# Optimization experiments

Hardware: AMD Instinct MI355X
Metric: run time of the kernel (lower is better)

## Reference

```python
import jax, jax.numpy as jnp
from jax import lax
import numpy as np

DIM = 800
FEAT = 192
LAYERS = 5
BLOCK_SZ = [32, 192, 192, 192, 192]
BLOCK_RNG = [0, 32, 224, 416, 608, 800]
HALF = 27  # image_size//4//2 - 1 with image_size=224
EPS = 1e-5


def conv2d(x, w, stride=1, pad=0, groups=1):
    return lax.conv_general_dilated(
        x, w, (stride, stride), [(pad, pad), (pad, pad)],
        dimension_numbers=("NCHW", "OIHW", "NCHW"),
        feature_group_count=groups)


def _bcast(v):
    return v[None, :, None, None]


def setup_inputs() -> dict:
    key = jax.random.key(0)
    ks = jax.random.split(key, 22)
    B = 32
    s = 0.05
    return {
        "x": jax.random.normal(ks[0], (B, 3, 224, 224), jnp.float32),
        "ds_w1": jax.random.normal(ks[1], (16, 3, 3, 3), jnp.float32) * s,
        "ds_b1": jax.random.normal(ks[2], (16,), jnp.float32) * s,
        "bn1_g": jax.random.uniform(ks[3], (16,), jnp.float32) + 0.5,
        "bn1_b": jax.random.normal(ks[4], (16,), jnp.float32) * s,
        "bn1_m": jax.random.normal(ks[5], (16,), jnp.float32) * s,
        "bn1_v": jax.random.uniform(ks[6], (16,), jnp.float32) + 0.5,
        "ds_dw": jax.random.normal(ks[7], (16, 1, 3, 3), jnp.float32) * s,
        "ds_dwb": jax.random.normal(ks[8], (16,), jnp.float32) * s,
        "ds_w2": jax.random.normal(ks[9], (32, 16, 1, 1), jnp.float32) * s,
        "ds_b2": jax.random.normal(ks[10], (32,), jnp.float32) * s,
        "bn2_g": jax.random.uniform(ks[11], (32,), jnp.float32) + 0.5,
        "bn2_b": jax.random.normal(ks[12], (32,), jnp.float32) * s,
        "bn2_m": jax.random.normal(ks[13], (32,), jnp.float32) * s,
        "bn2_v": jax.random.uniform(ks[14], (32,), jnp.float32) + 0.5,
        "conv_dw": jax.random.normal(ks[15], (DIM, 1, 3, 3), jnp.float32) * s,
        "gw": jax.random.normal(ks[16], (DIM, DIM), jnp.float32) * s,
        "in_gamma": jax.random.uniform(ks[17], (DIM,), jnp.float32) + 0.5,
        "in_beta": jax.random.normal(ks[18], (DIM,), jnp.float32) * s,
        "fc_w": jax.random.normal(ks[19], (1000, FEAT), jnp.float32) * s,
        "fc_b": jax.random.normal(ks[20], (1000,), jnp.float32) * s,
    }


def _forward(x, ds_w1, ds_b1, bn1_g, bn1_b, bn1_m, bn1_v, ds_dw, ds_dwb,
             ds_w2, ds_b2, bn2_g, bn2_b, bn2_m, bn2_v, conv_dw, gw,
             in_gamma, in_beta, fc_w, fc_b):
    # ---- downsample stem: conv3x3 s2 -> BN -> ReLU -> dwconv3x3 s2 -> conv1x1 -> BN
    h = conv2d(x, ds_w1, 2, 1) + _bcast(ds_b1)
    h = (h - _bcast(bn1_m)) * _bcast(bn1_g * lax.rsqrt(bn1_v + EPS)) + _bcast(bn1_b)
    h = jax.nn.relu(h)
    h = conv2d(h, ds_dw, 2, 1, groups=16) + _bcast(ds_dwb)
    h = conv2d(h, ds_w2, 1, 0) + _bcast(ds_b2)
    h = (h - _bcast(bn2_m)) * _bcast(bn2_g * lax.rsqrt(bn2_v + EPS)) + _bcast(bn2_b)
    B, _, H, W = h.shape  # (B, 32, 56, 56)
    h = jnp.concatenate([h, jnp.zeros((B, DIM - 32, H, W), h.dtype)], axis=1)

    # ---- per-block InstanceNorm -> ReLU -> depthwise conv -> sliced 1x1 graph conv -> residual
    for i in range(LAYERS):
        s, r0, r1 = BLOCK_SZ[i], BLOCK_RNG[i], BLOCK_RNG[i + 1]
        xa = h[:, :s]
        mu = xa.mean((2, 3), keepdims=True)
        var = ((xa - mu) ** 2).mean((2, 3), keepdims=True)
        xa = (xa - mu) * lax.rsqrt(var + EPS)
        xa = xa * _bcast(in_gamma[r0:r1]) + _bcast(in_beta[r0:r1])
        xa = jax.nn.relu(xa)
        xa = conv2d(xa, conv_dw[r0:r1], 1, 1, groups=s)
        row0 = min(r1, DIM - FEAT)
        xa = jnp.einsum("oc,bchw->bohw", gw[row0:, r0:r1], xa)
        h = (h[:, s:] if i < LAYERS - 1 else h[:, -FEAT:]) + xa

    # ---- AvgPool2d(2) over the 3x3 crop keeps only the top-left 2x2 mean
    out = h[:, :, HALF - 1:HALF + 1, HALF - 1:HALF + 1].mean((2, 3))
    return out @ fc_w.T + fc_b


def reference(x, ds_w1, ds_b1, bn1_g, bn1_b, bn1_m, bn1_v, ds_dw, ds_dwb,
              ds_w2, ds_b2, bn2_g, bn2_b, bn2_m, bn2_v, conv_dw, gw,
              in_gamma, in_beta, fc_w, fc_b):
    return _forward(x, ds_w1, ds_b1, bn1_g, bn1_b, bn1_m, bn1_v, ds_dw, ds_dwb,
                    ds_w2, ds_b2, bn2_g, bn2_b, bn2_m, bn2_v, conv_dw, gw,
                    in_gamma, in_beta, fc_w, fc_b)
```

## Files before the change

kernel.cpp:

```cpp
#include <hip/hip_runtime.h>
#include <stddef.h>

#define EPS 1e-5f
#define N_HW 3136
#define G 16
#define NG (G * N_HW)
#define DIMC 800

typedef unsigned short u16;
typedef __attribute__((ext_vector_type(8))) short short8;
typedef __attribute__((ext_vector_type(4))) float floatx4;

__device__ __forceinline__ u16 f2b(float f) {
  unsigned u = __float_as_uint(f);
  u += 0x7FFFu + ((u >> 16) & 1u);
  return (u16)(u >> 16);
}
__device__ __forceinline__ float blo(unsigned u) { return __uint_as_float(u << 16); }
__device__ __forceinline__ float bhi(unsigned u) { return __uint_as_float(u & 0xFFFF0000u); }

static const size_t XA_OFF  = 0;
static const size_t H0_OFF  = 61014016ull;
static const size_t BLK_OFF = 67436544ull;
static const size_t GWB_OFF = 105971712ull;
static const size_t M4_OFF  = 107251712ull;
static const size_t MH_OFF  = M4_OFF + 192 * G * 4;
static const size_t OP_OFF  = MH_OFF + 192 * G * 4;
static const size_t NEED    = OP_OFF + (size_t)G * 192 * 4;

__global__ __launch_bounds__(256) void gw2bf(const float* __restrict__ gw, u16* __restrict__ gwb) {
  int i = (blockIdx.x * 256 + threadIdx.x) * 4;
  float4 v = *(const float4*)(gw + i);
  gwb[i + 0] = f2b(v.x); gwb[i + 1] = f2b(v.y);
  gwb[i + 2] = f2b(v.z); gwb[i + 3] = f2b(v.w);
}

#define XT_PITCH 226
#define XT_CH (17 * XT_PITCH)
__global__ __launch_bounds__(256) void stem_conv1(
    const float* __restrict__ xg, const float* __restrict__ w, const float* __restrict__ b1,
    const float* __restrict__ g, const float* __restrict__ bb,
    const float* __restrict__ m, const float* __restrict__ v,
    float* __restrict__ h1) {
  __shared__ float xt[3 * XT_CH];
  __shared__ float wt[16 * 27];
  __shared__ float mulc[16], addc[16];
  int blk = blockIdx.x;
  int s = blk % 14;
  int bg = blk / 14;
  int tid = threadIdx.x;

  for (int e = tid; e < 432; e += 256) wt[e] = w[e];
  if (tid < 16) {
    float A = g[tid] * rsqrtf(v[tid] + EPS);
    mulc[tid] = A;
    addc[tid] = (b1[tid] - m[tid]) * A + bb[tid];
  }
  int iy0 = 16 * s - 1;
  for (int e = tid; e < 3 * XT_CH; e += 256) {
    int ci = e / XT_CH;
    int rem = e - ci * XT_CH;
    int r = rem / XT_PITCH;
    int cc = rem - r * XT_PITCH;
    int iy = iy0 + r, ix = cc - 1;
    float val = 0.f;
    if (iy >= 0 && iy < 224 && ix >= 0 && ix < 224)
      val = xg[((size_t)(bg * 3 + ci)) * 224 * 224 + iy * 224 + ix];
    xt[e] = val;
  }
  __syncthreads();

  for (int p = tid; p < 8 * 112; p += 256) {
    int oyl = p / 112, ox = p - oyl * 112;
    float xv[27];
#pragma unroll
    for (int ci = 0; ci < 3; ci++)
#pragma unroll
      for (int ky = 0; ky < 3; ky++)
#pragma unroll
        for (int kx = 0; kx < 3; kx++)
          xv[ci * 9 + ky * 3 + kx] = xt[ci * XT_CH + (2 * oyl + ky) * XT_PITCH + 2 * ox + kx];
    int oy = 8 * s + oyl;
#pragma unroll
    for (int c = 0; c < 16; c++) {
      float acc = 0.f;
#pragma unroll
      for (int t = 0; t < 27; t++) acc += xv[t] * wt[c * 27 + t];
      float y = acc * mulc[c] + addc[c];
      h1[(size_t)(c * G + bg) * 12544 + oy * 112 + ox] = fmaxf(y, 0.f);
    }
  }
}

__global__ __launch_bounds__(256) void stem_dw(
    const float* __restrict__ h1, const float* __restrict__ dw, const float* __restrict__ dwb,
    float* __restrict__ h2) {
  int idx = blockIdx.x * 256 + threadIdx.x;
  int q = idx % N_HW;
  int t = idx / N_HW;
  int bg = t & (G - 1);
  int c = t >> 4;
  int qy = q / 56, qx = q % 56;
  const float* plane = h1 + (size_t)(c * G + bg) * 12544;
  float acc = dwb[c];
#pragma unroll
  for (int ky = 0; ky < 3; ky++) {
    int iy = qy * 2 - 1 + ky;
    if (iy < 0 || iy >= 112) continue;
#pragma unroll
    for (int kx = 0; kx < 3; kx++) {
      int ix = qx * 2 - 1 + kx;
      if (ix < 0 || ix >= 112) continue;
      acc += plane[iy * 112 + ix] * dw[c * 9 + ky * 3 + kx];
    }
  }
  h2[idx] = acc;
}

__global__ __launch_bounds__(256) void stem_pw(
    const float* __restrict__ h2, const float* __restrict__ w2, const float* __restrict__ b2,
    const float* __restrict__ g, const float* __restrict__ bb,
    const float* __restrict__ m, const float* __restrict__ v,
    float* __restrict__ H0) {
  int idx = blockIdx.x * 256 + threadIdx.x;
  int q = idx % N_HW;
  int t = idx / N_HW;
  int bg = t & (G - 1);
  int o = t >> 4;
  float acc = b2[o];
#pragma unroll
  for (int c = 0; c < 16; c++) acc += w2[o * 16 + c] * h2[(size_t)(c * G + bg) * N_HW + q];
  float y = (acc - m[o]) * (g[o] * rsqrtf(v[o] + EPS)) + bb[o];
  H0[idx] = y;
}

template <typename T>
__global__ __launch_bounds__(256) void dw_fused(
    const T* __restrict__ base, const float* __restrict__ cdw,
    const float* __restrict__ in_g, const float* __restrict__ in_b,
    u16* __restrict__ XA, int cdwoff) {
  __shared__ float sm[58 * 58];
  __shared__ float wred[8];
  int blk = blockIdx.x;
  int cl = blk >> 4;
  int c = cdwoff + cl;
  int tid = threadIdx.x;

  if (tid < 58) { sm[tid] = 0.f; sm[57 * 58 + tid] = 0.f; }
  if (tid >= 64 && tid < 120) { int r = tid - 63; sm[r * 58] = 0.f; sm[r * 58 + 57] = 0.f; }

  const T* row = base + (size_t)blk * N_HW;
  float s = 0.f, s2 = 0.f;
  for (int i = tid; i < 392; i += 256) {
    float vals[8];
    if constexpr (sizeof(T) == 2) {
      uint4 u = *(const uint4*)((const u16*)row + i * 8);
      vals[0] = blo(u.x); vals[1] = bhi(u.x);
      vals[2] = blo(u.y); vals[3] = bhi(u.y);
      vals[4] = blo(u.z); vals[5] = bhi(u.z);
      vals[6] = blo(u.w); vals[7] = bhi(u.w);
    } else {
      float4 v0 = *(const float4*)((const float*)row + i * 8);
      float4 v1 = *(const float4*)((const float*)row + i * 8 + 4);
      vals[0] = v0.x; vals[1] = v0.y; vals[2] = v0.z; vals[3] = v0.w;
      vals[4] = v1.x; vals[5] = v1.y; vals[6] = v1.z; vals[7] = v1.w;
    }
    int p = i * 8;
    int y = p / 56, x = p - y * 56;
    float* d = &sm[(y + 1) * 58 + x + 1];
#pragma unroll
    for (int e = 0; e < 8; e++) {
      d[e] = vals[e];
      s += vals[e];
      s2 += vals[e] * vals[e];
    }
  }
#pragma unroll
  for (int o = 32; o > 0; o >>= 1) {
    s += __shfl_down(s, o);
    s2 += __shfl_down(s2, o);
  }
  if ((tid & 63) == 0) { wred[(tid >> 6) * 2] = s; wred[(tid >> 6) * 2 + 1] = s2; }
  __syncthreads();
  float ts = (wred[0] + wred[2]) + (wred[4] + wred[6]);
  float tq = (wred[1] + wred[3]) + (wred[5] + wred[7]);
  float mean = ts * (1.f / N_HW);
  float var = fmaxf(tq * (1.f / N_HW) - mean * mean, 0.f);
  float sc = in_g[c] * rsqrtf(var + EPS);
  float sh = in_b[c] - mean * sc;

  for (int i = tid; i < N_HW; i += 256) {
    int y = i / 56, x = i - y * 56;
    int pos = (y + 1) * 58 + x + 1;
    sm[pos] = fmaxf(sm[pos] * sc + sh, 0.f);
  }
  __syncthreads();

  float w0 = cdw[c * 9 + 0], w1 = cdw[c * 9 + 1], w2 = cdw[c * 9 + 2];
  float w3 = cdw[c * 9 + 3], w4 = cdw[c * 9 + 4], w5 = cdw[c * 9 + 5];
  float w6 = cdw[c * 9 + 6], w7 = cdw[c * 9 + 7], w8 = cdw[c * 9 + 8];
  u16* outp = XA + (size_t)blk * N_HW;
  for (int pp = tid; pp < N_HW / 2; pp += 256) {
    int p = pp * 2;
    int y = p / 56, x = p - y * 56;
    const float* p0 = &sm[y * 58 + x];
    float a0 = p0[0] * w0 + p0[1] * w1 + p0[2] * w2
             + p0[58] * w3 + p0[59] * w4 + p0[60] * w5
             + p0[116] * w6 + p0[117] * w7 + p0[118] * w8;
    float a1 = p0[1] * w0 + p0[2] * w1 + p0[3] * w2
             + p0[59] * w3 + p0[60] * w4 + p0[61] * w5
             + p0[117] * w6 + p0[118] * w7 + p0[119] * w8;
    unsigned pk = (unsigned)f2b(a0) | ((unsigned)f2b(a1) << 16);
    *(unsigned*)&outp[p] = pk;
  }
}

template <typename TC>
__global__ __launch_bounds__(256) void gemm_mfma(
    const u16* __restrict__ A, const u16* __restrict__ B, TC* __restrict__ C, int K) {
  __shared__ u16 As[2][192][40];
  __shared__ u16 Bs[2][32][64];
  int n0 = blockIdx.x * 64;
  int tid = threadIdx.x;
  int wave = tid >> 6, lane = tid & 63;
  int wm = wave >> 1, wn = wave & 1;
  int lg = lane >> 4, li = lane & 15;
  floatx4 acc[6][2] = {};

  int ar = tid >> 2, ak = (tid & 3) * 8;
  int bk = tid >> 3, bn = (tid & 7) * 8;
  int bnx = bn ^ ((bk >> 3) << 4);
  const u16* Ag = A + (size_t)ar * DIMC + ak;
  const u16* Bg = B + (size_t)bk * NG + n0 + bn;

  int nt = K / 32;
  *(uint4*)&As[0][ar][ak]       = *(const uint4*)(Ag);
  *(uint4*)&As[0][ar + 64][ak]  = *(const uint4*)(Ag + (size_t)64 * DIMC);
  *(uint4*)&As[0][ar + 128][ak] = *(const uint4*)(Ag + (size_t)128 * DIMC);
  *(uint4*)&Bs[0][bk][bnx]      = *(const uint4*)(Bg);
  __syncthreads();

  int cur = 0;
  for (int t = 0; t < nt; t++) {
    uint4 ra0, ra1, ra2, rb;
    bool pf = (t + 1 < nt);
    if (pf) {
      const u16* ag = Ag + (size_t)(t + 1) * 32;
      ra0 = *(const uint4*)(ag);
      ra1 = *(const uint4*)(ag + (size_t)64 * DIMC);
      ra2 = *(const uint4*)(ag + (size_t)128 * DIMC);
      rb  = *(const uint4*)(Bg + (size_t)(t + 1) * 32 * NG);
    }
    short8 aF[6];
#pragma unroll
    for (int mi = 0; mi < 6; mi++)
      aF[mi] = *(const short8*)&As[cur][wm * 96 + mi * 16 + li][lg * 8];
#pragma unroll
    for (int ni = 0; ni < 2; ni++) {
      int colx = ((wn * 32 + ni * 16) ^ (lg << 4)) + li;
      short8 bF;
#pragma unroll
      for (int e = 0; e < 8; e++) bF[e] = (short)Bs[cur][lg * 8 + e][colx];
#pragma unroll
      for (int mi = 0; mi < 6; mi++)
        acc[mi][ni] = __builtin_amdgcn_mfma_f32_16x16x32_bf16(aF[mi], bF, acc[mi][ni], 0, 0, 0);
    }
    if (pf) {
      *(uint4*)&As[cur ^ 1][ar][ak]       = ra0;
      *(uint4*)&As[cur ^ 1][ar + 64][ak]  = ra1;
      *(uint4*)&As[cur ^ 1][ar + 128][ak] = ra2;
      *(uint4*)&Bs[cur ^ 1][bk][bnx]      = rb;
    }
    __syncthreads();
    cur ^= 1;
  }

#pragma unroll
  for (int mi = 0; mi < 6; mi++) {
#pragma unroll
    for (int ni = 0; ni < 2; ni++) {
      int row = wm * 96 + mi * 16 + lg * 4;
      int col = n0 + wn * 32 + ni * 16 + li;
      TC* cp = C + (size_t)row * NG + col;
#pragma unroll
      for (int r = 0; r < 4; r++) {
        if constexpr (sizeof(TC) == 2) cp[(size_t)r * NG] = f2b(acc[mi][ni][r]);
        else                           cp[(size_t)r * NG] = acc[mi][ni][r];
      }
    }
  }
}

__global__ __launch_bounds__(256) void head_m4(
    const float* __restrict__ HT, const float* __restrict__ in_g, const float* __restrict__ in_b,
    const float* __restrict__ cdw, float* __restrict__ m4, float* __restrict__ meanH) {
  int blk = blockIdx.x;
  int cl = blk >> 4;
  int c = 608 + cl;
  int tid = threadIdx.x;
  const float* row = HT + (size_t)blk * N_HW;
  float s = 0.f, s2 = 0.f;
  for (int i = tid; i < N_HW; i += 256) {
    float xv = row[i];
    s += xv; s2 += xv * xv;
  }
  __shared__ float red[256], red2[256];
  red[tid] = s; red2[tid] = s2;
  __syncthreads();
  for (int o = 128; o > 0; o >>= 1) {
    if (tid < o) { red[tid] += red[tid + o]; red2[tid] += red2[tid + o]; }
    __syncthreads();
  }
  if (tid == 0) {
    float mean = red[0] * (1.f / N_HW);
    float var = fmaxf(red2[0] * (1.f / N_HW) - mean * mean, 0.f);
    float sc = in_g[c] * rsqrtf(var + EPS);
    float sh = in_b[c] - mean * sc;
    float val[4][4];
#pragma unroll
    for (int dy = 0; dy < 4; dy++)
#pragma unroll
      for (int dx = 0; dx < 4; dx++)
        val[dy][dx] = fmaxf(row[(25 + dy) * 56 + 25 + dx] * sc + sh, 0.f);
    const float* w = cdw + c * 9;
    float acc = 0.f;
#pragma unroll
    for (int oy = 1; oy < 3; oy++)
#pragma unroll
      for (int ox = 1; ox < 3; ox++)
#pragma unroll
        for (int ky = 0; ky < 3; ky++)
#pragma unroll
          for (int kx = 0; kx < 3; kx++)
            acc += val[oy + ky - 1][ox + kx - 1] * w[ky * 3 + kx];
    m4[blk] = acc * 0.25f;
    meanH[blk] = 0.25f * (row[26 * 56 + 26] + row[26 * 56 + 27] +
                          row[27 * 56 + 26] + row[27 * 56 + 27]);
  }
}

__global__ __launch_bounds__(256) void head_mix(
    const float* __restrict__ gw, const float* __restrict__ m4, const float* __restrict__ meanH,
    float* __restrict__ out_pre) {
  int idx = blockIdx.x * 256 + threadIdx.x;
  if (idx >= G * 192) return;
  int j = idx % 192;
  int bg = idx / 192;
  float acc = meanH[j * G + bg];
  const float* grow = gw + (size_t)(608 + j) * DIMC + 608;
  for (int c = 0; c < 192; c++) acc += grow[c] * m4[c * G + bg];
  out_pre[idx] = acc;
}

__global__ __launch_bounds__(256) void head_fc(
    const float* __restrict__ out_pre, const float* __restrict__ fc_w,
    const float* __restrict__ fc_b, float* __restrict__ outg) {
  int idx = blockIdx.x * 256 + threadIdx.x;
  if (idx >= G * 1000) return;
  int t = idx % 1000;
  int bg = idx / 1000;
  float acc = fc_b[t];
  const float* wr = fc_w + (size_t)t * 192;
  const float* hr = out_pre + (size_t)bg * 192;
  for (int j = 0; j < 192; j++) acc += wr[j] * hr[j];
  outg[idx] = acc;
}

extern "C" void kernel_launch(void* const* d_in, const int* in_sizes, int n_in,
                              void* d_out, int out_size, void* d_ws, size_t ws_size,
                              hipStream_t stream) {
  const float* x      = (const float*)d_in[0];
  const float* ds_w1  = (const float*)d_in[1];
  const float* ds_b1  = (const float*)d_in[2];
  const float* bn1_g  = (const float*)d_in[3];
  const float* bn1_b  = (const float*)d_in[4];
  const float* bn1_m  = (const float*)d_in[5];
  const float* bn1_v  = (const float*)d_in[6];
  const float* ds_dw  = (const float*)d_in[7];
  const float* ds_dwb = (const float*)d_in[8];
  const float* ds_w2  = (const float*)d_in[9];
  const float* ds_b2  = (const float*)d_in[10];
  const float* bn2_g  = (const float*)d_in[11];
  const float* bn2_b  = (const float*)d_in[12];
  const float* bn2_m  = (const float*)d_in[13];
  const float* bn2_v  = (const float*)d_in[14];
  const float* cdw    = (const float*)d_in[15];
  const float* gw     = (const float*)d_in[16];
  const float* in_g   = (const float*)d_in[17];
  const float* in_b   = (const float*)d_in[18];
  const float* fc_w   = (const float*)d_in[19];
  const float* fc_b   = (const float*)d_in[20];
  float* out = (float*)d_out;
  char* ws = (char*)d_ws;

  if (ws_size < NEED) return;

  u16*   XAc    = (u16*)(ws + XA_OFF);
  float* H0     = (float*)(ws + H0_OFF);
  u16*   blockb = (u16*)(ws + BLK_OFF);
  float* blockf = (float*)(ws + BLK_OFF);
  u16*   gwb    = (u16*)(ws + GWB_OFF);
  float* m4     = (float*)(ws + M4_OFF);
  float* meanH  = (float*)(ws + MH_OFF);
  float* opre   = (float*)(ws + OP_OFF);
  float* h1     = (float*)(ws + BLK_OFF);
  float* h2     = h1 + (size_t)16 * G * 12544;

  gw2bf<<<625, 256, 0, stream>>>(gw, gwb);

  static const int CDWOFF[4] = {0, 32, 224, 416};
  static const int SZ[4]     = {32, 192, 192, 192};
  static const int RA[4]     = {32, 224, 416, 608};
  static const int KK[4]     = {32, 224, 416, 608};

  for (int g = 0; g < 32 / G; g++) {
    const float* xg = x + (size_t)g * G * 3 * 224 * 224;

    stem_conv1<<<14 * G, 256, 0, stream>>>(
        xg, ds_w1, ds_b1, bn1_g, bn1_b, bn1_m, bn1_v, h1);
    stem_dw<<<16 * G * N_HW / 256, 256, 0, stream>>>(h1, ds_dw, ds_dwb, h2);
    stem_pw<<<32 * G * N_HW / 256, 256, 0, stream>>>(
        h2, ds_w2, ds_b2, bn2_g, bn2_b, bn2_m, bn2_v, H0);

    for (int i = 0; i < 4; i++) {
      if (i == 0)
        dw_fused<float><<<SZ[i] * G, 256, 0, stream>>>(
            H0, cdw, in_g, in_b, XAc + (size_t)CDWOFF[i] * NG, CDWOFF[i]);
      else
        dw_fused<u16><<<SZ[i] * G, 256, 0, stream>>>(
            blockb, cdw, in_g, in_b, XAc + (size_t)CDWOFF[i] * NG, CDWOFF[i]);
      if (i < 3)
        gemm_mfma<u16><<<NG / 64, 256, 0, stream>>>(
            gwb + (size_t)RA[i] * DIMC, XAc, blockb, KK[i]);
      else
        gemm_mfma<float><<<NG / 64, 256, 0, stream>>>(
            gwb + (size_t)RA[i] * DIMC, XAc, blockf, KK[i]);
    }

    head_m4<<<192 * G, 256, 0, stream>>>(blockf, in_g, in_b, cdw, m4, meanH);
    head_mix<<<(G * 192 + 255) / 256, 256, 0, stream>>>(gw, m4, meanH, opre);
    head_fc<<<(G * 1000 + 255) / 256, 256, 0, stream>>>(opre, fc_w, fc_b, out + (size_t)g * G * 1000);
  }
}
```

Measured before the change: 428.7 us.

## Process full batch at once and fuse last-layer stats into GEMM epilogue

Raises the batch group from 16 to 32 so each stage runs as one launch over the whole batch, halving the number of kernel launches and giving larger grids. The last GEMM no longer writes the full fp32 output; its epilogue instead reduces per-channel sums and squared sums with shuffles and atomics, and stores only the 3 spatial tiles needed by the center crop. head_m4 then becomes a small elementwise kernel reading these stats and patch values. This adds atomic contention and a stats-zeroing launch, and doubles workspace size.

```diff
diff --git a/kernel.cpp b/kernel.cpp
--- a/kernel.cpp
+++ b/kernel.cpp
@@ -3,9 +3,10 @@
 
 #define EPS 1e-5f
 #define N_HW 3136
-#define G 16
+#define G 32
 #define NG (G * N_HW)
 #define DIMC 800
+#define NTILE 49
 
 typedef unsigned short u16;
 typedef __attribute__((ext_vector_type(8))) short short8;
@@ -20,19 +21,26 @@
 __device__ __forceinline__ float bhi(unsigned u) { return __uint_as_float(u & 0xFFFF0000u); }
 
 static const size_t XA_OFF  = 0;
-static const size_t H0_OFF  = 61014016ull;
-static const size_t BLK_OFF = 67436544ull;
-static const size_t GWB_OFF = 105971712ull;
-static const size_t M4_OFF  = 107251712ull;
-static const size_t MH_OFF  = M4_OFF + 192 * G * 4;
-static const size_t OP_OFF  = MH_OFF + 192 * G * 4;
-static const size_t NEED    = OP_OFF + (size_t)G * 192 * 4;
+static const size_t H0_OFF  = 122028032ull;
+static const size_t BLK_OFF = 134873088ull;
+static const size_t GWB_OFF = 173408256ull;
+static const size_t STS_OFF = 174688256ull;
+static const size_t STQ_OFF = 174712832ull;
+static const size_t PAT_OFF = 174737408ull;
+static const size_t M4_OFF  = 179456000ull;
+static const size_t MH_OFF  = M4_OFF + 6144 * 4;
+static const size_t OP_OFF  = MH_OFF + 6144 * 4;
+static const size_t NEED    = OP_OFF + 6144 * 4;
 
 __global__ __launch_bounds__(256) void gw2bf(const float* __restrict__ gw, u16* __restrict__ gwb) {
   int i = (blockIdx.x * 256 + threadIdx.x) * 4;
   float4 v = *(const float4*)(gw + i);
   gwb[i + 0] = f2b(v.x); gwb[i + 1] = f2b(v.y);
   gwb[i + 2] = f2b(v.z); gwb[i + 3] = f2b(v.w);
+}
+
+__global__ __launch_bounds__(256) void zero_stats(float* __restrict__ p) {
+  p[blockIdx.x * 256 + threadIdx.x] = 0.f;
 }
 
 #define XT_PITCH 226
@@ -99,7 +107,7 @@
   int q = idx % N_HW;
   int t = idx / N_HW;
   int bg = t & (G - 1);
-  int c = t >> 4;
+  int c = t >> 5;
   int qy = q / 56, qx = q % 56;
   const float* plane = h1 + (size_t)(c * G + bg) * 12544;
   float acc = dwb[c];
@@ -126,7 +134,7 @@
   int q = idx % N_HW;
   int t = idx / N_HW;
   int bg = t & (G - 1);
-  int o = t >> 4;
+  int o = t >> 5;
   float acc = b2[o];
 #pragma unroll
   for (int c = 0; c < 16; c++) acc += w2[o * 16 + c] * h2[(size_t)(c * G + bg) * N_HW + q];
@@ -142,7 +150,7 @@
   __shared__ float sm[58 * 58];
   __shared__ float wred[8];
   int blk = blockIdx.x;
-  int cl = blk >> 4;
+  int cl = blk >> 5;
   int c = cdwoff + cl;
   int tid = threadIdx.x;
 
@@ -215,9 +223,11 @@
   }
 }
 
-template <typename TC>
+template <int MODE>
 __global__ __launch_bounds__(256) void gemm_mfma(
-    const u16* __restrict__ A, const u16* __restrict__ B, TC* __restrict__ C, int K) {
+    const u16* __restrict__ A, const u16* __restrict__ B, u16* __restrict__ C,
+    float* __restrict__ statS, float* __restrict__ statQ, float* __restrict__ patchf,
+    int K) {
   __shared__ u16 As[2][192][40];
   __shared__ u16 Bs[2][32][64];
   int n0 = blockIdx.x * 64;
@@ -275,68 +285,100 @@
     cur ^= 1;
   }
 
-#pragma unroll
-  for (int mi = 0; mi < 6; mi++) {
-#pragma unroll
-    for (int ni = 0; ni < 2; ni++) {
-      int row = wm * 96 + mi * 16 + lg * 4;
-      int col = n0 + wn * 32 + ni * 16 + li;
-      TC* cp = C + (size_t)row * NG + col;
+  if constexpr (MODE == 0) {
+#pragma unroll
+    for (int mi = 0; mi < 6; mi++) {
+#pragma unroll
+      for (int ni = 0; ni < 2; ni++) {
+        int row = wm * 96 + mi * 16 + lg * 4;
+        int col = n0 + wn * 32 + ni * 16 + li;
+        u16* cp = C + (size_t)row * NG + col;
+#pragma unroll
+        for (int r = 0; r < 4; r++) cp[(size_t)r * NG] = f2b(acc[mi][ni][r]);
+      }
+    }
+  } else {
+    int bg = blockIdx.x / NTILE;
+    int tile = blockIdx.x % NTILE;
+#pragma unroll
+    for (int mi = 0; mi < 6; mi++) {
 #pragma unroll
       for (int r = 0; r < 4; r++) {
-        if constexpr (sizeof(TC) == 2) cp[(size_t)r * NG] = f2b(acc[mi][ni][r]);
-        else                           cp[(size_t)r * NG] = acc[mi][ni][r];
+        float v0 = acc[mi][0][r], v1 = acc[mi][1][r];
+        float s = v0 + v1;
+        float q = v0 * v0 + v1 * v1;
+#pragma unroll
+        for (int msk = 1; msk < 16; msk <<= 1) {
+          s += __shfl_xor(s, msk);
+          q += __shfl_xor(q, msk);
+        }
+        if (li == 0) {
+          int row = wm * 96 + mi * 16 + lg * 4 + r;
+          atomicAdd(&statS[row * 32 + bg], s);
+          atomicAdd(&statQ[row * 32 + bg], q);
+        }
       }
     }
+    if (tile >= 22 && tile <= 24) {
+#pragma unroll
+      for (int mi = 0; mi < 6; mi++) {
+#pragma unroll
+        for (int ni = 0; ni < 2; ni++) {
+          int row = wm * 96 + mi * 16 + lg * 4;
+          int pc = (tile - 22) * 64 + wn * 32 + ni * 16 + li;
+#pragma unroll
+          for (int r = 0; r < 4; r++)
+            patchf[((size_t)(row + r) * 32 + bg) * 192 + pc] = acc[mi][ni][r];
+        }
+      }
+    }
   }
 }
 
 __global__ __launch_bounds__(256) void head_m4(
-    const float* __restrict__ HT, const float* __restrict__ in_g, const float* __restrict__ in_b,
+    const float* __restrict__ statS, const float* __restrict__ statQ,
+    const float* __restrict__ patchf,
+    const float* __restrict__ in_g, const float* __restrict__ in_b,
     const float* __restrict__ cdw, float* __restrict__ m4, float* __restrict__ meanH) {
-  int blk = blockIdx.x;
-  int cl = blk >> 4;
+  int idx = blockIdx.x * 256 + threadIdx.x;
+  if (idx >= 192 * 32) return;
+  int cl = idx >> 5;
   int c = 608 + cl;
-  int tid = threadIdx.x;
-  const float* row = HT + (size_t)blk * N_HW;
-  float s = 0.f, s2 = 0.f;
-  for (int i = tid; i < N_HW; i += 256) {
-    float xv = row[i];
-    s += xv; s2 += xv * xv;
-  }
-  __shared__ float red[256], red2[256];
-  red[tid] = s; red2[tid] = s2;
-  __syncthreads();
-  for (int o = 128; o > 0; o >>= 1) {
-    if (tid < o) { red[tid] += red[tid + o]; red2[tid] += red2[tid + o]; }
-    __syncthreads();
-  }
-  if (tid == 0) {
-    float mean = red[0] * (1.f / N_HW);
-    float var = fmaxf(red2[0] * (1.f / N_HW) - mean * mean, 0.f);
-    float sc = in_g[c] * rsqrtf(var + EPS);
-    float sh = in_b[c] - mean * sc;
-    float val[4][4];
-#pragma unroll
-    for (int dy = 0; dy < 4; dy++)
-#pragma unroll
-      for (int dx = 0; dx < 4; dx++)
-        val[dy][dx] = fmaxf(row[(25 + dy) * 56 + 25 + dx] * sc + sh, 0.f);
-    const float* w = cdw + c * 9;
-    float acc = 0.f;
-#pragma unroll
-    for (int oy = 1; oy < 3; oy++)
-#pragma unroll
-      for (int ox = 1; ox < 3; ox++)
-#pragma unroll
-        for (int ky = 0; ky < 3; ky++)
-#pragma unroll
-          for (int kx = 0; kx < 3; kx++)
-            acc += val[oy + ky - 1][ox + kx - 1] * w[ky * 3 + kx];
-    m4[blk] = acc * 0.25f;
-    meanH[blk] = 0.25f * (row[26 * 56 + 26] + row[26 * 56 + 27] +
-                          row[27 * 56 + 26] + row[27 * 56 + 27]);
-  }
+  float mean = statS[idx] * (1.f / N_HW);
+  float var = fmaxf(statQ[idx] * (1.f / N_HW) - mean * mean, 0.f);
+  float sc = in_g[c] * rsqrtf(var + EPS);
+  float sh = in_b[c] - mean * sc;
+  const float* pf = patchf + (size_t)idx * 192;
+  float val[4][4];
+#pragma unroll
+  for (int dy = 0; dy < 4; dy++)
+#pragma unroll
+    for (int dx = 0; dx < 4; dx++) {
+      int hw = (25 + dy) * 56 + 25 + dx;
+      float v = pf[((hw >> 6) - 22) * 64 + (hw & 63)];
+      val[dy][dx] = fmaxf(v * sc + sh, 0.f);
+    }
+  const float* w = cdw + c * 9;
+  float acc = 0.f;
+#pragma unroll
+  for (int oy = 1; oy < 3; oy++)
+#pragma unroll
+    for (int ox = 1; ox < 3; ox++)
+#pragma unroll
+      for (int ky = 0; ky < 3; ky++)
+#pragma unroll
+        for (int kx = 0; kx < 3; kx++)
+          acc += val[oy + ky - 1][ox + kx - 1] * w[ky * 3 + kx];
+  m4[idx] = acc * 0.25f;
+  float mh = 0.f;
+#pragma unroll
+  for (int dy = 0; dy < 2; dy++)
+#pragma unroll
+    for (int dx = 0; dx < 2; dx++) {
+      int hw = (26 + dy) * 56 + 26 + dx;
+      mh += pf[((hw >> 6) - 22) * 64 + (hw & 63)];
+    }
+  meanH[idx] = mh * 0.25f;
 }
 
 __global__ __launch_bounds__(256) void head_mix(
@@ -398,8 +440,10 @@
   u16*   XAc    = (u16*)(ws + XA_OFF);
   float* H0     = (float*)(ws + H0_OFF);
   u16*   blockb = (u16*)(ws + BLK_OFF);
-  float* blockf = (float*)(ws + BLK_OFF);
   u16*   gwb    = (u16*)(ws + GWB_OFF);
+  float* statS  = (float*)(ws + STS_OFF);
+  float* statQ  = (float*)(ws + STQ_OFF);
+  float* patchf = (float*)(ws + PAT_OFF);
   float* m4     = (float*)(ws + M4_OFF);
   float* meanH  = (float*)(ws + MH_OFF);
   float* opre   = (float*)(ws + OP_OFF);
@@ -407,38 +451,35 @@
   float* h2     = h1 + (size_t)16 * G * 12544;
 
   gw2bf<<<625, 256, 0, stream>>>(gw, gwb);
+  zero_stats<<<48, 256, 0, stream>>>(statS);
 
   static const int CDWOFF[4] = {0, 32, 224, 416};
   static const int SZ[4]     = {32, 192, 192, 192};
   static const int RA[4]     = {32, 224, 416, 608};
   static const int KK[4]     = {32, 224, 416, 608};
 
-  for (int g = 0; g < 32 / G; g++) {
-    const float* xg = x + (size_t)g * G * 3 * 224 * 224;
-
-    stem_conv1<<<14 * G, 256, 0, stream>>>(
-        xg, ds_w1, ds_b1, bn1_g, bn1_b, bn1_m, bn1_v, h1);
-    stem_dw<<<16 * G * N_HW / 256, 256, 0, stream>>>(h1, ds_dw, ds_dwb, h2);
-    stem_pw<<<32 * G * N_HW / 256, 256, 0, stream>>>(
-        h2, ds_w2, ds_b2, bn2_g, bn2_b, bn2_m, bn2_v, H0);
-
-    for (int i = 0; i < 4; i++) {
-      if (i == 0)
-        dw_fused<float><<<SZ[i] * G, 256, 0, stream>>>(
-            H0, cdw, in_g, in_b, XAc + (size_t)CDWOFF[i] * NG, CDWOFF[i]);
-      else
-        dw_fused<u16><<<SZ[i] * G, 256, 0, stream>>>(
-            blockb, cdw, in_g, in_b, XAc + (size_t)CDWOFF[i] * NG, CDWOFF[i]);
-      if (i < 3)
-        gemm_mfma<u16><<<NG / 64, 256, 0, stream>>>(
-            gwb + (size_t)RA[i] * DIMC, XAc, blockb, KK[i]);
-      else
-        gemm_mfma<float><<<NG / 64, 256, 0, stream>>>(
-            gwb + (size_t)RA[i] * DIMC, XAc, blockf, KK[i]);
-    }
-
-    head_m4<<<192 * G, 256, 0, stream>>>(blockf, in_g, in_b, cdw, m4, meanH);
-    head_mix<<<(G * 192 + 255) / 256, 256, 0, stream>>>(gw, m4, meanH, opre);
-    head_fc<<<(G * 1000 + 255) / 256, 256, 0, stream>>>(opre, fc_w, fc_b, out + (size_t)g * G * 1000);
-  }
-}
+  stem_conv1<<<14 * G, 256, 0, stream>>>(
+      x, ds_w1, ds_b1, bn1_g, bn1_b, bn1_m, bn1_v, h1);
+  stem_dw<<<16 * G * N_HW / 256, 256, 0, stream>>>(h1, ds_dw, ds_dwb, h2);
+  stem_pw<<<32 * G * N_HW / 256, 256, 0, stream>>>(
+      h2, ds_w2, ds_b2, bn2_g, bn2_b, bn2_m, bn2_v, H0);
+
+  for (int i = 0; i < 4; i++) {
+    if (i == 0)
+      dw_fused<float><<<SZ[i] * G, 256, 0, stream>>>(
+          H0, cdw, in_g, in_b, XAc + (size_t)CDWOFF[i] * NG, CDWOFF[i]);
+    else
+      dw_fused<u16><<<SZ[i] * G, 256, 0, stream>>>(
+          blockb, cdw, in_g, in_b, XAc + (size_t)CDWOFF[i] * NG, CDWOFF[i]);
+    if (i < 3)
+      gemm_mfma<0><<<NG / 64, 256, 0, stream>>>(
+          gwb + (size_t)RA[i] * DIMC, XAc, blockb, nullptr, nullptr, nullptr, KK[i]);
+    else
+      gemm_mfma<1><<<NG / 64, 256, 0, stream>>>(
+          gwb + (size_t)RA[i] * DIMC, XAc, nullptr, statS, statQ, patchf, KK[i]);
+  }
+
+  head_m4<<<24, 256, 0, stream>>>(statS, statQ, patchf, in_g, in_b, cdw, m4, meanH);
+  head_mix<<<(G * 192 + 255) / 256, 256, 0, stream>>>(gw, m4, meanH, opre);
+  head_fc<<<(G * 1000 + 255) / 256, 256, 0, stream>>>(opre, fc_w, fc_b, out);
+}
```

Measured after the change: 392.2 us. 1.09x faster.
